# Kernel tuning notes

Measured on AMD Instinct MI355X. Metric: run time of the kernel, lower is better.

The kernel has to match this reference:

```python
import jax, jax.numpy as jnp
import numpy as np

B, Q, L, D = 4, 600, 2048, 256
H, HD, DFF, KD = 8, 32, 2048, 32  # heads, head_dim, ffn dim, gasa kernel dim
SCALE = HD ** -0.5


def setup_inputs() -> dict:
    key = jax.random.key(0)
    ks = jax.random.split(key, 24)
    w = lambda k, shape, s=0.02: (jax.random.normal(k, shape, jnp.float32) * s)
    inp = {
        "queries": jax.random.normal(ks[0], (B, Q, D), jnp.float32),
        "memory": jax.random.normal(ks[1], (B, L, D), jnp.float32),
        "memory_pos": jax.random.normal(ks[2], (B, L, 3), jnp.float32),
        "query_pos": jax.random.normal(ks[3], (B, Q, 3), jnp.float32),
        # self-attention (nn.MultiheadAttention packed in_proj)
        "sa_in_w": w(ks[4], (3 * D, D)), "sa_in_b": jnp.zeros((3 * D,), jnp.float32),
        "sa_out_w": w(ks[5], (D, D)), "sa_out_b": jnp.zeros((D,), jnp.float32),
        "norm1_g": jnp.ones((D,), jnp.float32), "norm1_b": jnp.zeros((D,), jnp.float32),
        # cross-attention projections
        "q_w": w(ks[6], (D, D)), "q_b": jnp.zeros((D,), jnp.float32),
        "k_w": w(ks[7], (D, D)), "k_b": jnp.zeros((D,), jnp.float32),
        "v_w": w(ks[8], (D, D)), "v_b": jnp.zeros((D,), jnp.float32),
        "o_w": w(ks[9], (D, D)), "o_b": jnp.zeros((D,), jnp.float32),
        "norm2_g": jnp.ones((D,), jnp.float32), "norm2_b": jnp.zeros((D,), jnp.float32),
        # GASA geometric-bias kernel: beta, MLP 1->KD->1
        "beta": jnp.asarray(1.0, jnp.float32),
        "dk_w1": w(ks[10], (KD, 1), 0.1), "dk_b1": jnp.zeros((KD,), jnp.float32),
        "dk_w2": w(ks[11], (1, KD), 0.1), "dk_b2": jnp.full((1,), -1.0, jnp.float32),
        # FFN
        "ffn_w1": w(ks[12], (DFF, D)), "ffn_b1": jnp.zeros((DFF,), jnp.float32),
        "ffn_w2": w(ks[13], (D, DFF)), "ffn_b2": jnp.zeros((D,), jnp.float32),
        "norm3_g": jnp.ones((D,), jnp.float32), "norm3_b": jnp.zeros((D,), jnp.float32),
    }
    return inp


def _ln(x, g, b, eps=1e-5):
    m = jnp.mean(x, -1, keepdims=True)
    v = jnp.mean((x - m) ** 2, -1, keepdims=True)
    return (x - m) * jax.lax.rsqrt(v + eps) * g + b


def _heads(x, wt, b):  # x:[B,N,D] -> [B,H,N,HD]
    y = x @ wt.T + b
    return y.reshape(x.shape[0], x.shape[1], H, HD).transpose(0, 2, 1, 3)


def reference(queries, memory, memory_pos, query_pos,
              sa_in_w, sa_in_b, sa_out_w, sa_out_b, norm1_g, norm1_b,
              q_w, q_b, k_w, k_b, v_w, v_b, o_w, o_b, norm2_g, norm2_b,
              beta, dk_w1, dk_b1, dk_w2, dk_b2,
              ffn_w1, ffn_b1, ffn_w2, ffn_b2, norm3_g, norm3_b):
    # ---- self-attention (post-norm, no query_pe) ----
    wq, wk, wv = jnp.split(sa_in_w, 3, axis=0)
    bq, bk, bv = jnp.split(sa_in_b, 3)
    qh = _heads(queries, wq, bq)
    kh = _heads(queries, wk, bk)
    vh = _heads(queries, wv, bv)
    a = jax.nn.softmax(jnp.einsum('bhqd,bhkd->bhqk', qh, kh) * SCALE, axis=-1)
    sa = jnp.einsum('bhqk,bhkd->bhqd', a, vh).transpose(0, 2, 1, 3).reshape(B, Q, D)
    sa = sa @ sa_out_w.T + sa_out_b
    x = _ln(queries + sa, norm1_g, norm1_b)

    # ---- GASA cross-attention ----
    Qh = _heads(x, q_w, q_b)          # [B,H,Q,HD]
    Kh = _heads(memory, k_w, k_b)     # [B,H,L,HD]
    Vh = _heads(memory, v_w, v_b)     # [B,H,L,HD]
    # cdist + learned kernel MLP, clamp to [-10, 0] (suppress-only)
    d2 = jnp.sum((query_pos[:, :, None, :] - memory_pos[:, None, :, :]) ** 2, -1)
    dist = jnp.sqrt(jnp.maximum(d2, 0.0))                     # [B,Q,L]
    hid = jax.nn.relu(dist[..., None] * dk_w1[:, 0] + dk_b1)  # [B,Q,L,KD]
    bias = (hid @ dk_w2[0]) + dk_b2[0]                        # [B,Q,L]
    bias = jnp.clip(bias, -10.0, 0.0)
    scores = jnp.einsum('bhqd,bhkd->bhqk', Qh, Kh) * SCALE + beta * bias[:, None]
    attn = jax.nn.softmax(scores, axis=-1)
    ca = jnp.einsum('bhqk,bhkd->bhqd', attn, Vh).transpose(0, 2, 1, 3).reshape(B, Q, D)
    ca = ca @ o_w.T + o_b
    x = _ln(x + ca, norm2_g, norm2_b)

    # ---- FFN (post-norm) ----
    f = jax.nn.relu(x @ ffn_w1.T + ffn_b1) @ ffn_w2.T + ffn_b2
    return _ln(x + f, norm3_g, norm3_b)
```

## Files before the change

kernel.cpp:

```cpp
#include <hip/hip_runtime.h>
#include <hip/hip_bf16.h>

typedef __hip_bfloat16 bf16;
typedef __attribute__((ext_vector_type(8))) short  short8;
typedef __attribute__((ext_vector_type(4))) short  short4v;
typedef __attribute__((ext_vector_type(4))) float  f32x4;

#define B_ 4
#define Q_ 600
#define L_ 2048
#define D_ 256
#define H_ 8
#define HD_ 32
#define DFF_ 2048
#define KD_ 32
#define SCALE_ 0.17677669529663687f
#define L2E_   1.4426950408889634f
#define SL2E_  (SCALE_ * L2E_)

template<int MODE>
__device__ __forceinline__ float ldx(const void* p, size_t i, bool f32)
{
    if (MODE == 0) return __bfloat162float(((const bf16*)p)[i]);
    if (MODE == 1) return ((const float*)p)[i];
    return f32 ? ((const float*)p)[i] : __bfloat162float(((const bf16*)p)[i]);
}
__device__ __forceinline__ short8 ld8_f32(const float* p)
{
    const float4 a = *(const float4*)p;
    const float4 b = *(const float4*)(p + 4);
    union { short8 s; bf16 h[8]; } u;
    u.h[0] = __float2bfloat16(a.x); u.h[1] = __float2bfloat16(a.y);
    u.h[2] = __float2bfloat16(a.z); u.h[3] = __float2bfloat16(a.w);
    u.h[4] = __float2bfloat16(b.x); u.h[5] = __float2bfloat16(b.y);
    u.h[6] = __float2bfloat16(b.z); u.h[7] = __float2bfloat16(b.w);
    return u.s;
}
template<int MODE>
__device__ __forceinline__ short8 ld8x(const void* p, size_t i, bool f32)
{
    if (MODE == 0) return *(const short8*)((const bf16*)p + i);
    if (MODE == 1) return ld8_f32((const float*)p + i);
    return f32 ? ld8_f32((const float*)p + i) : *(const short8*)((const bf16*)p + i);
}

__global__ __launch_bounds__(256)
void detect_kernel(const unsigned short* __restrict__ q, int* __restrict__ flag)
{
    __shared__ float red[4];
    const int tid = threadIdx.x;
    unsigned short u = q[tid];
    float f = __uint_as_float(((unsigned)(u & 0x7FFF)) << 16);
    if (f != f) f = 1e30f;
    #pragma unroll
    for (int o = 32; o > 0; o >>= 1) f = fmaxf(f, __shfl_xor(f, o));
    if ((tid & 63) == 0) red[tid >> 6] = f;
    __syncthreads();
    if (tid == 0) {
        float m = fmaxf(fmaxf(red[0], red[1]), fmaxf(red[2], red[3]));
        *flag = (m > 100.f) ? 1 : 0;
    }
}

template<int AM>
__device__ __forceinline__ void gemm_core(const void* __restrict__ A,
    const void* __restrict__ W, int M, int K, int kbeg, int kend,
    int bm, int bn, bool f32, bf16* As, bf16* Bs, f32x4 (&acc)[2][2])
{
    const int tid = threadIdx.x;
    const int w = tid >> 6, lane = tid & 63;
    const int quad = lane >> 4, l16 = lane & 15;
    const int wm = (w & 1) << 5, wn = (w >> 1) << 5;
    const int srow = tid >> 2, scol = (tid & 3) << 3;
    const int gma = (bm + srow < M) ? bm + srow : M - 1;

    short8 pa = ld8x<AM>(A, (size_t)gma * K + kbeg + scol, f32);
    short8 pb = ld8x<2>(W, (size_t)(bn + srow) * K + kbeg + scol, f32);

    for (int k0 = kbeg; k0 < kend; k0 += 32) {
        *(short8*)&As[srow * 40 + scol] = pa;
        *(short8*)&Bs[srow * 40 + scol] = pb;
        __syncthreads();
        if (k0 + 32 < kend) {
            pa = ld8x<AM>(A, (size_t)gma * K + k0 + 32 + scol, f32);
            pb = ld8x<2>(W, (size_t)(bn + srow) * K + k0 + 32 + scol, f32);
        }
        short8 af[2], bfr[2];
        #pragma unroll
        for (int t = 0; t < 2; t++) {
            af[t]  = *(const short8*)&As[(wm + t * 16 + l16) * 40 + quad * 8];
            bfr[t] = *(const short8*)&Bs[(wn + t * 16 + l16) * 40 + quad * 8];
        }
        #pragma unroll
        for (int mt = 0; mt < 2; mt++)
            #pragma unroll
            for (int nt = 0; nt < 2; nt++)
                acc[mt][nt] = __builtin_amdgcn_mfma_f32_16x16x32_bf16(
                    af[mt], bfr[nt], acc[mt][nt], 0, 0, 0);
        __syncthreads();
    }
}

template<int AM, int RM, int CM, bool RELU, int SPLIT>
__global__ __launch_bounds__(256)
void gemm_mfma(const void* __restrict__ A, const void* __restrict__ W,
               const void* __restrict__ bias, const void* __restrict__ R,
               void* __restrict__ C, int M, int N, int K,
               const int* __restrict__ flagp)
{
    const bool f32 = (*flagp != 0);
    __shared__ alignas(16) bf16 As[64 * 40];
    __shared__ alignas(16) bf16 Bs[64 * 40];
    const int bm = blockIdx.y << 6, bn = blockIdx.x << 6;
    const int KS = K / SPLIT, z = (SPLIT > 1) ? blockIdx.z : 0;

    f32x4 acc[2][2] = {{{0.f,0.f,0.f,0.f},{0.f,0.f,0.f,0.f}},
                       {{0.f,0.f,0.f,0.f},{0.f,0.f,0.f,0.f}}};
    gemm_core<AM>(A, W, M, K, z * KS, z * KS + KS, bm, bn, f32, As, Bs, acc);

    const int tid = threadIdx.x;
    const int w = tid >> 6, lane = tid & 63;
    const int quad = lane >> 4, l16 = lane & 15;
    const int wm = (w & 1) << 5, wn = (w >> 1) << 5;

    #pragma unroll
    for (int mt = 0; mt < 2; mt++) {
        #pragma unroll
        for (int r = 0; r < 4; r++) {
            const int row = bm + wm + mt * 16 + quad * 4 + r;
            if (row >= M) continue;
            #pragma unroll
            for (int nt = 0; nt < 2; nt++) {
                const int col = bn + wn + nt * 16 + l16;
                if (SPLIT > 1) {
                    ((float*)C)[((size_t)z * M + row) * N + col] = acc[mt][nt][r];
                } else {
                    float v = acc[mt][nt][r] + ldx<2>(bias, col, f32);
                    if (RM >= 0) v += ldx<RM < 0 ? 0 : RM>(R, (size_t)row * N + col, f32);
                    if (RELU) v = fmaxf(v, 0.f);
                    if (CM == 0) ((bf16*)C)[(size_t)row * N + col] = __float2bfloat16(v);
                    else         ((float*)C)[(size_t)row * N + col] = v;
                }
            }
        }
    }
}

__global__ __launch_bounds__(256)
void kv_proj(const void* __restrict__ A,
             const void* __restrict__ kw, const void* __restrict__ kb,
             const void* __restrict__ vw, const void* __restrict__ vb,
             bf16* __restrict__ kf, bf16* __restrict__ vf,
             int M, int K, const int* __restrict__ flagp)
{
    const bool f32 = (*flagp != 0);
    __shared__ alignas(16) bf16 As[64 * 40];
    __shared__ alignas(16) bf16 Bs[64 * 40];
    const int sel = blockIdx.x >> 2;
    const void* W  = sel ? vw : kw;
    const void* bs = sel ? vb : kb;
    bf16* C        = sel ? vf : kf;
    const int bn = (blockIdx.x & 3) << 6;
    const int bm = blockIdx.y << 6;

    f32x4 acc[2][2] = {{{0.f,0.f,0.f,0.f},{0.f,0.f,0.f,0.f}},
                       {{0.f,0.f,0.f,0.f},{0.f,0.f,0.f,0.f}}};
    gemm_core<2>(A, W, M, K, 0, K, bm, bn, f32, As, Bs, acc);

    const int tid = threadIdx.x;
    const int w = tid >> 6, lane = tid & 63;
    const int quad = lane >> 4, l16 = lane & 15;
    const int wm = (w & 1) << 5, wn = (w >> 1) << 5;
    #pragma unroll
    for (int mt = 0; mt < 2; mt++)
        #pragma unroll
        for (int r = 0; r < 4; r++) {
            const int row = bm + wm + mt * 16 + quad * 4 + r;
            if (row >= M) continue;
            #pragma unroll
            for (int nt = 0; nt < 2; nt++) {
                const int col = bn + wn + nt * 16 + l16;
                C[(size_t)row * 256 + col] =
                    __float2bfloat16(acc[mt][nt][r] + ldx<2>(bs, col, f32));
            }
        }
}

template<int RM, int OM, int S>
__global__ __launch_bounds__(64)
void red_ln(const float* __restrict__ P, const void* __restrict__ bias,
            const void* __restrict__ R, const void* __restrict__ gg,
            const void* __restrict__ bb, void* __restrict__ Y,
            int M, const int* __restrict__ flagp)
{
    const bool f32 = (*flagp != 0);
    const int row = blockIdx.x, lane = threadIdx.x;
    const int d0 = lane * 4;
    float v[4];
    {
        float4 a = *(const float4*)(P + ((size_t)0 * M + row) * D_ + d0);
        v[0] = a.x; v[1] = a.y; v[2] = a.z; v[3] = a.w;
    }
    #pragma unroll
    for (int s = 1; s < S; s++) {
        float4 a = *(const float4*)(P + ((size_t)s * M + row) * D_ + d0);
        v[0] += a.x; v[1] += a.y; v[2] += a.z; v[3] += a.w;
    }
    #pragma unroll
    for (int j = 0; j < 4; j++)
        v[j] += ldx<2>(bias, d0 + j, f32) + ldx<RM>(R, (size_t)row * D_ + d0 + j, f32);

    float s1 = v[0] + v[1] + v[2] + v[3];
    float s2 = v[0]*v[0] + v[1]*v[1] + v[2]*v[2] + v[3]*v[3];
    #pragma unroll
    for (int o = 32; o > 0; o >>= 1) {
        s1 += __shfl_xor(s1, o);
        s2 += __shfl_xor(s2, o);
    }
    const float mean = s1 * (1.f / D_);
    const float var = s2 * (1.f / D_) - mean * mean;
    const float rinv = rsqrtf(var + 1e-5f);
    float o[4];
    #pragma unroll
    for (int j = 0; j < 4; j++)
        o[j] = (v[j] - mean) * rinv * ldx<2>(gg, d0 + j, f32) + ldx<2>(bb, d0 + j, f32);
    const size_t i = (size_t)row * D_ + d0;
    if (OM == 1 || (OM == 2 && f32)) {
        float4 t{o[0], o[1], o[2], o[3]};
        *(float4*)((float*)Y + i) = t;
    } else {
        bf16* y = (bf16*)Y + i;
        y[0] = __float2bfloat16(o[0]); y[1] = __float2bfloat16(o[1]);
        y[2] = __float2bfloat16(o[2]); y[3] = __float2bfloat16(o[3]);
    }
}

template<bool HASBIAS, int NSEG>
__global__ __launch_bounds__(256)
void flash_attn(const bf16* __restrict__ Qm, int qs,
                const bf16* __restrict__ Km, int ks,
                const bf16* __restrict__ Vm, int vs,
                const bf16* __restrict__ biasT,
                bf16* __restrict__ pO, float* __restrict__ pml,
                int NQ, int LK)
{
    __shared__ alignas(16) bf16 Ksh[64 * 40];
    __shared__ alignas(16) bf16 Vt[48 * 72];
    __shared__ alignas(16) bf16 Psh[64 * 72];
    __shared__ alignas(16) bf16 Bsh[HASBIAS ? 64 * 72 : 8];

    const int tid = threadIdx.x;
    const int w = tid >> 6, lane = tid & 63;
    const int quad = lane >> 4, l16 = lane & 15;

    const int id = blockIdx.x;
    const int g  = ((id >> 6) << 3) + (id & 7);
    const int h  = (id >> 3) & 7;
    const int qt = g % 10;
    const int zz = g / 10;
    const int b = zz & 3, seg = zz >> 2;
    const int q0 = qt * 64;
    const int segLen = LK / NSEG;
    const int lbeg = seg * segLen, lend = lbeg + segLen;

    for (int i = tid; i < 16 * 72; i += 256) {
        int rr = 32 + i / 72, cc = i % 72;
        Vt[rr * 72 + cc] = __float2bfloat16(rr == 32 ? 1.f : 0.f);
    }

    int qrow = q0 + w * 16 + l16; if (qrow > NQ - 1) qrow = NQ - 1;
    const short8 aq = *(const short8*)(Qm + (size_t)(b * NQ + qrow) * qs + h * HD_ + quad * 8);

    f32x4 O0 = {0.f,0.f,0.f,0.f}, O1 = {0.f,0.f,0.f,0.f}, O2 = {0.f,0.f,0.f,0.f};

    const int srow = tid >> 2, sc4 = tid & 3;
    const int nch = (segLen + 63) >> 6;

    for (int ch = 0; ch < nch; ch++) {
        const int l0 = lbeg + (ch << 6);
        {
            int lg = l0 + srow; if (lg > LK - 1) lg = LK - 1;
            short8 k8 = *(const short8*)(Km + (size_t)(b * LK + lg) * ks + h * HD_ + sc4 * 8);
            *(short8*)&Ksh[srow * 40 + sc4 * 8] = k8;
            short8 v8 = *(const short8*)(Vm + (size_t)(b * LK + lg) * vs + h * HD_ + sc4 * 8);
            const int swc = srow ^ (sc4 * 16);
            #pragma unroll
            for (int j = 0; j < 8; j++)
                Vt[(sc4 * 8 + j) * 72 + swc] = ((const bf16*)&v8)[j];
            if (HASBIAS) {
                #pragma unroll
                for (int rep = 0; rep < 2; rep++) {
                    int chid = tid + rep * 256;
                    int ll = chid >> 3, qc = chid & 7;
                    int qread = q0 + qc * 8;
                    if (qread > NQ - 8) qread = NQ - 8;
                    *(short8*)&Bsh[ll * 72 + qc * 8] =
                        *(const short8*)(biasT + ((size_t)(b * LK) + l0 + ll) * Q_ + qread);
                }
            }
        }
        __syncthreads();

        f32x4 sv[4];
        #pragma unroll
        for (int jt = 0; jt < 4; jt++) {
            short8 kb = *(const short8*)&Ksh[(jt * 16 + l16) * 40 + quad * 8];
            sv[jt] = __builtin_amdgcn_mfma_f32_16x16x32_bf16(aq, kb, (f32x4){0.f,0.f,0.f,0.f}, 0, 0, 0);
        }
        if (l0 + 64 <= lend) {
            #pragma unroll
            for (int jt = 0; jt < 4; jt++) {
                if (HASBIAS) {
                    short4v bb = *(const short4v*)&Bsh[(jt * 16 + l16) * 72 + w * 16 + quad * 4];
                    #pragma unroll
                    for (int r = 0; r < 4; r++)
                        Psh[(w * 16 + quad * 4 + r) * 72 + jt * 16 + l16] =
                            __float2bfloat16(exp2f(sv[jt][r] * SL2E_ +
                                __bfloat162float(((const bf16*)&bb)[r])));
                } else {
                    #pragma unroll
                    for (int r = 0; r < 4; r++)
                        Psh[(w * 16 + quad * 4 + r) * 72 + jt * 16 + l16] =
                            __float2bfloat16(exp2f(sv[jt][r] * SL2E_));
                }
            }
        } else {
            #pragma unroll
            for (int jt = 0; jt < 4; jt++) {
                const bool valid = (l0 + jt * 16 + l16) < lend;
                #pragma unroll
                for (int r = 0; r < 4; r++)
                    Psh[(w * 16 + quad * 4 + r) * 72 + jt * 16 + l16] =
                        __float2bfloat16(valid ? exp2f(sv[jt][r] * SL2E_) : 0.f);
            }
        }
        __syncthreads();
        const int sw0 = 16 * (l16 >> 3);
        const int sw1 = 16 * (2 + (l16 >> 3));
        #pragma unroll
        for (int kt = 0; kt < 2; kt++) {
            short8 ap  = *(const short8*)&Psh[(w * 16 + l16) * 72 + kt * 32 + quad * 8];
            short8 bv0 = *(const short8*)&Vt[(l16) * 72 + ((kt * 32 + quad * 8) ^ sw0)];
            short8 bv1 = *(const short8*)&Vt[(16 + l16) * 72 + ((kt * 32 + quad * 8) ^ sw1)];
            short8 bon = *(const short8*)&Vt[(32 + l16) * 72 + kt * 32 + quad * 8];
            O0 = __builtin_amdgcn_mfma_f32_16x16x32_bf16(ap, bv0, O0, 0, 0, 0);
            O1 = __builtin_amdgcn_mfma_f32_16x16x32_bf16(ap, bv1, O1, 0, 0, 0);
            O2 = __builtin_amdgcn_mfma_f32_16x16x32_bf16(ap, bon, O2, 0, 0, 0);
        }
        __syncthreads();
    }

    #pragma unroll
    for (int r = 0; r < 4; r++) {
        const int qg = q0 + w * 16 + quad * 4 + r;
        if (qg >= NQ) continue;
        const float li = __shfl(O2[r], lane & 48);
        const float inv = 1.f / li;
        const size_t rowp = (size_t)(((seg * 4 + b) * 8) + h) * NQ + qg;
        bf16* op = pO + rowp * 32;
        op[l16]      = __float2bfloat16(O0[r] * inv);
        op[16 + l16] = __float2bfloat16(O1[r] * inv);
        if (l16 == 0) { pml[rowp * 2 + 0] = 0.f; pml[rowp * 2 + 1] = O2[r]; }
    }
}

template<int NSEG>
__global__ __launch_bounds__(256)
void attn_combine(const bf16* __restrict__ pO, const float* __restrict__ pml,
                  bf16* __restrict__ ctx, int NQ)
{
    const int t = blockIdx.x * 256 + threadIdx.x;
    const int row = t >> 5, d = t & 31;
    const int stride = 32 * NQ;
    float ms[NSEG], ls[NSEG];
    float M = -3e38f;
    #pragma unroll
    for (int s = 0; s < NSEG; s++) {
        ms[s] = pml[(size_t)(s * stride + row) * 2 + 0];
        ls[s] = pml[(size_t)(s * stride + row) * 2 + 1];
        M = fmaxf(M, ms[s]);
    }
    float W = 0.f, acc = 0.f;
    #pragma unroll
    for (int s = 0; s < NSEG; s++) {
        float wgt = ls[s] * exp2f(ms[s] - M);
        W += wgt;
        acc += wgt * __bfloat162float(pO[(size_t)(s * stride + row) * 32 + d]);
    }
    const int bh = row / NQ, q = row - bh * NQ;
    ctx[((size_t)((bh >> 3) * NQ + q)) * D_ + (bh & 7) * HD_ + d] = __float2bfloat16(acc / W);
}

__global__ __launch_bounds__(256)
void bias_pre(const void* __restrict__ qp, const void* __restrict__ mp,
              const void* __restrict__ w1, const void* __restrict__ b1,
              const void* __restrict__ w2, const void* __restrict__ b2,
              const void* __restrict__ betap, bf16* __restrict__ out,
              const int* __restrict__ flagp)
{
    const bool f32 = (*flagp != 0);
    __shared__ float sw1[KD_], sb1[KD_], sw2[KD_], scst[2];
    const int tid = threadIdx.x;
    if (tid < KD_) {
        sw1[tid] = ldx<2>(w1, tid, f32);
        sb1[tid] = ldx<2>(b1, tid, f32);
        sw2[tid] = ldx<2>(w2, tid, f32);
    }
    if (tid == 0) { scst[0] = ldx<2>(b2, 0, f32); scst[1] = L2E_ * ldx<2>(betap, 0, f32); }
    __syncthreads();
    const int idx = blockIdx.x * 256 + tid;
    const int q8 = idx % 75;
    const int t2 = idx / 75;
    const int l = t2 % L_, b = t2 / L_;
    const int q0 = q8 * 8;
    const float mx = ldx<2>(mp, (size_t)(b * L_ + l) * 3 + 0, f32);
    const float my = ldx<2>(mp, (size_t)(b * L_ + l) * 3 + 1, f32);
    const float mz = ldx<2>(mp, (size_t)(b * L_ + l) * 3 + 2, f32);
    union { short8 s; bf16 h[8]; } res;
    #pragma unroll
    for (int j = 0; j < 8; j++) {
        const int q = q0 + j;
        float dx = ldx<2>(qp, (size_t)(b * Q_ + q) * 3 + 0, f32) - mx;
        float dy = ldx<2>(qp, (size_t)(b * Q_ + q) * 3 + 1, f32) - my;
        float dz = ldx<2>(qp, (size_t)(b * Q_ + q) * 3 + 2, f32) - mz;
        float dist = sqrtf(dx * dx + dy * dy + dz * dz);
        float acc = scst[0];
        #pragma unroll
        for (int k = 0; k < KD_; k++)
            acc += fmaxf(dist * sw1[k] + sb1[k], 0.f) * sw2[k];
        acc = fminf(fmaxf(acc, -10.f), 0.f);
        res.h[j] = __float2bfloat16(scst[1] * acc);
    }
    *(short8*)(out + ((size_t)(b * L_) + l) * Q_ + q0) = res.s;
}

extern "C" void kernel_launch(void* const* d_in, const int* in_sizes, int n_in,
                              void* d_out, int out_size, void* d_ws, size_t ws_size,
                              hipStream_t stream)
{
    const void* queries   = d_in[0];
    const void* memory    = d_in[1];
    const void* memory_pos= d_in[2];
    const void* query_pos = d_in[3];
    const void* sa_in_w   = d_in[4];
    const void* sa_in_b   = d_in[5];
    const void* sa_out_w  = d_in[6];
    const void* sa_out_b  = d_in[7];
    const void* norm1_g   = d_in[8];
    const void* norm1_b   = d_in[9];
    const void* q_w  = d_in[10], *q_b  = d_in[11];
    const void* k_w  = d_in[12], *k_b  = d_in[13];
    const void* v_w  = d_in[14], *v_b  = d_in[15];
    const void* o_w  = d_in[16], *o_b  = d_in[17];
    const void* norm2_g = d_in[18], *norm2_b = d_in[19];
    const void* beta  = d_in[20];
    const void* dk_w1 = d_in[21], *dk_b1 = d_in[22];
    const void* dk_w2 = d_in[23], *dk_b2 = d_in[24];
    const void* ffn_w1 = d_in[25], *ffn_b1 = d_in[26];
    const void* ffn_w2 = d_in[27], *ffn_b2 = d_in[28];
    const void* norm3_g = d_in[29], *norm3_b = d_in[30];

    char* base = (char*)d_ws;
    bf16*  kf     = (bf16*)(base + 0);
    bf16*  vf     = (bf16*)(base + 4194304);
    float* x1     = (float*)(base + 8388608);
    bf16*  qproj  = (bf16*)(base + 10846208);
    bf16*  cactx  = (bf16*)(base + 12075008);
    float* x2     = (float*)(base + 13303808);
    bf16*  biasT  = (bf16*)(base + 15761408);
    bf16*  qkv    = (bf16*)(base + 0);
    bf16*  sactx  = (bf16*)(base + 3686400);
    bf16*  selfO  = (bf16*)(base + 4915200);
    float* selfML = (float*)(base + 7372800);
    float* P3     = (float*)(base + 15761408);
    bf16*  crossO = (bf16*)(base + 25591808);
    float* crossML= (float*)(base + 30507008);
    float* P10    = (float*)(base + 0);
    bf16*  ffnh   = (bf16*)(base + 15761408);
    float* P13    = (float*)(base + 0);
    int*   flag   = (int*)(base + 31121408);

    const dim3 blk(256);

    detect_kernel<<<1, 256, 0, stream>>>((const unsigned short*)queries, flag);
    gemm_mfma<2, -1, 0, false, 1><<<dim3(12, 38), blk, 0, stream>>>(
        queries, sa_in_w, sa_in_b, nullptr, qkv, 2400, 768, 256, flag);
    flash_attn<false, 2><<<640, blk, 0, stream>>>(
        qkv, 768, qkv + 256, 768, qkv + 512, 768, nullptr,
        selfO, selfML, 600, 600);
    attn_combine<2><<<2400, blk, 0, stream>>>(selfO, selfML, sactx, 600);
    gemm_mfma<0, -1, 1, false, 2><<<dim3(4, 38, 2), blk, 0, stream>>>(
        sactx, sa_out_w, nullptr, nullptr, P3, 2400, 256, 256, flag);
    red_ln<2, 1, 2><<<2400, 64, 0, stream>>>(
        P3, sa_out_b, queries, norm1_g, norm1_b, x1, 2400, flag);
    gemm_mfma<1, -1, 0, false, 1><<<dim3(4, 38), blk, 0, stream>>>(
        x1, q_w, q_b, nullptr, qproj, 2400, 256, 256, flag);
    kv_proj<<<dim3(8, 128), blk, 0, stream>>>(
        memory, k_w, k_b, v_w, v_b, kf, vf, 8192, 256, flag);
    bias_pre<<<2400, blk, 0, stream>>>(
        query_pos, memory_pos, dk_w1, dk_b1, dk_w2, dk_b2, beta, biasT, flag);
    flash_attn<true, 4><<<1280, blk, 0, stream>>>(
        qproj, 256, kf, 256, vf, 256, biasT,
        crossO, crossML, 600, 2048);
    attn_combine<4><<<2400, blk, 0, stream>>>(crossO, crossML, cactx, 600);
    gemm_mfma<0, -1, 1, false, 2><<<dim3(4, 38, 2), blk, 0, stream>>>(
        cactx, o_w, nullptr, nullptr, P10, 2400, 256, 256, flag);
    red_ln<1, 1, 2><<<2400, 64, 0, stream>>>(
        P10, o_b, x1, norm2_g, norm2_b, x2, 2400, flag);
    gemm_mfma<1, -1, 0, true, 1><<<dim3(32, 38), blk, 0, stream>>>(
        x2, ffn_w1, ffn_b1, nullptr, ffnh, 2400, 2048, 256, flag);
    gemm_mfma<0, -1, 1, false, 4><<<dim3(4, 38, 4), blk, 0, stream>>>(
        ffnh, ffn_w2, nullptr, nullptr, P13, 2400, 256, 2048, flag);
    red_ln<1, 2, 4><<<2400, 64, 0, stream>>>(
        P13, ffn_b2, x2, norm3_g, norm3_b, d_out, 2400, flag);
}
```

Before: 292.3 us.

## Fuse split-attention combine into out-proj GEMM and merge independent prologue kernels

The attn_combine kernels are removed. The out-projection GEMMs now read the per-segment flash-attention partial outputs and merge them while loading their A operand, weighting each segment by its stored l and dropping the max term. The self-attn QKV projection, the K/V projection and the geometric-bias precompute are merged into one stage0 launch with a block-range dispatch, and the workspace layout is reassigned so these buffers can coexist. This cuts launch count and one round trip of the context tensor through memory. In exchange, the GEMM A-load redoes the combine for every N-tile, and correctness now relies on flash_attn normalising partials so that the per-segment max terms can be ignored.

```diff
diff --git a/kernel.cpp b/kernel.cpp
--- a/kernel.cpp
+++ b/kernel.cpp
@@ -44,6 +44,34 @@
     return f32 ? ld8_f32((const float*)p + i) : *(const short8*)((const bf16*)p + i);
 }
 
+template<int NSEG>
+__device__ __forceinline__ short8 ld8_comb(const bf16* __restrict__ pO,
+                                           const float* __restrict__ pml,
+                                           int row, int col)
+{
+    const unsigned b = (unsigned)row / 600u;
+    const unsigned q = (unsigned)row - b * 600u;
+    const int h = col >> 5, dd = col & 31;
+    const unsigned rp = b * 4800u + (unsigned)h * 600u + q;
+    float W = 0.f;
+    float acc[8] = {0.f,0.f,0.f,0.f,0.f,0.f,0.f,0.f};
+    #pragma unroll
+    for (int s = 0; s < NSEG; s++) {
+        const size_t rr = (size_t)s * 19200u + rp;
+        const float l = pml[rr * 2 + 1];
+        W += l;
+        const short8 o = *(const short8*)(pO + rr * 32 + dd);
+        #pragma unroll
+        for (int j = 0; j < 8; j++)
+            acc[j] += l * __bfloat162float(((const bf16*)&o)[j]);
+    }
+    const float inv = 1.f / W;
+    union { short8 s; bf16 h8[8]; } u;
+    #pragma unroll
+    for (int j = 0; j < 8; j++) u.h8[j] = __float2bfloat16(acc[j] * inv);
+    return u.s;
+}
+
 __global__ __launch_bounds__(256)
 void detect_kernel(const unsigned short* __restrict__ q, int* __restrict__ flag)
 {
@@ -62,10 +90,11 @@
     }
 }
 
-template<int AM>
+template<int AM, int NSEG>
 __device__ __forceinline__ void gemm_core(const void* __restrict__ A,
     const void* __restrict__ W, int M, int K, int kbeg, int kend,
-    int bm, int bn, bool f32, bf16* As, bf16* Bs, f32x4 (&acc)[2][2])
+    int bm, int bn, bool f32, bf16* As, bf16* Bs, f32x4 (&acc)[2][2],
+    const float* __restrict__ pml)
 {
     const int tid = threadIdx.x;
     const int w = tid >> 6, lane = tid & 63;
@@ -74,15 +103,18 @@
     const int srow = tid >> 2, scol = (tid & 3) << 3;
     const int gma = (bm + srow < M) ? bm + srow : M - 1;
 
-    short8 pa = ld8x<AM>(A, (size_t)gma * K + kbeg + scol, f32);
-    short8 pb = ld8x<2>(W, (size_t)(bn + srow) * K + kbeg + scol, f32);
+    short8 pa, pb;
+    if constexpr (AM == 3) pa = ld8_comb<NSEG>((const bf16*)A, pml, gma, kbeg + scol);
+    else                   pa = ld8x<AM>(A, (size_t)gma * K + kbeg + scol, f32);
+    pb = ld8x<2>(W, (size_t)(bn + srow) * K + kbeg + scol, f32);
 
     for (int k0 = kbeg; k0 < kend; k0 += 32) {
         *(short8*)&As[srow * 40 + scol] = pa;
         *(short8*)&Bs[srow * 40 + scol] = pb;
         __syncthreads();
         if (k0 + 32 < kend) {
-            pa = ld8x<AM>(A, (size_t)gma * K + k0 + 32 + scol, f32);
+            if constexpr (AM == 3) pa = ld8_comb<NSEG>((const bf16*)A, pml, gma, k0 + 32 + scol);
+            else                   pa = ld8x<AM>(A, (size_t)gma * K + k0 + 32 + scol, f32);
             pb = ld8x<2>(W, (size_t)(bn + srow) * K + k0 + 32 + scol, f32);
         }
         short8 af[2], bfr[2];
@@ -101,12 +133,40 @@
     }
 }
 
-template<int AM, int RM, int CM, bool RELU, int SPLIT>
+template<int RM, int CM, bool RELU>
+__device__ __forceinline__ void gemm_epi(const f32x4 (&acc)[2][2],
+    const void* __restrict__ bias, const void* __restrict__ R,
+    void* __restrict__ C, int M, int N, int bm, int bn, bool f32)
+{
+    const int tid = threadIdx.x;
+    const int w = tid >> 6, lane = tid & 63;
+    const int quad = lane >> 4, l16 = lane & 15;
+    const int wm = (w & 1) << 5, wn = (w >> 1) << 5;
+    #pragma unroll
+    for (int mt = 0; mt < 2; mt++) {
+        #pragma unroll
+        for (int r = 0; r < 4; r++) {
+            const int row = bm + wm + mt * 16 + quad * 4 + r;
+            if (row >= M) continue;
+            #pragma unroll
+            for (int nt = 0; nt < 2; nt++) {
+                const int col = bn + wn + nt * 16 + l16;
+                float v = acc[mt][nt][r] + ldx<2>(bias, col, f32);
+                if (RM >= 0) v += ldx<(RM < 0 ? 0 : RM)>(R, (size_t)row * N + col, f32);
+                if (RELU) v = fmaxf(v, 0.f);
+                if (CM == 0) ((bf16*)C)[(size_t)row * N + col] = __float2bfloat16(v);
+                else         ((float*)C)[(size_t)row * N + col] = v;
+            }
+        }
+    }
+}
+
+template<int AM, int RM, int CM, bool RELU, int SPLIT, int NSEG>
 __global__ __launch_bounds__(256)
 void gemm_mfma(const void* __restrict__ A, const void* __restrict__ W,
                const void* __restrict__ bias, const void* __restrict__ R,
                void* __restrict__ C, int M, int N, int K,
-               const int* __restrict__ flagp)
+               const int* __restrict__ flagp, const float* __restrict__ pml)
 {
     const bool f32 = (*flagp != 0);
     __shared__ alignas(16) bf16 As[64 * 40];
@@ -116,122 +176,105 @@
 
     f32x4 acc[2][2] = {{{0.f,0.f,0.f,0.f},{0.f,0.f,0.f,0.f}},
                        {{0.f,0.f,0.f,0.f},{0.f,0.f,0.f,0.f}}};
-    gemm_core<AM>(A, W, M, K, z * KS, z * KS + KS, bm, bn, f32, As, Bs, acc);
-
-    const int tid = threadIdx.x;
-    const int w = tid >> 6, lane = tid & 63;
-    const int quad = lane >> 4, l16 = lane & 15;
-    const int wm = (w & 1) << 5, wn = (w >> 1) << 5;
-
-    #pragma unroll
-    for (int mt = 0; mt < 2; mt++) {
-        #pragma unroll
-        for (int r = 0; r < 4; r++) {
-            const int row = bm + wm + mt * 16 + quad * 4 + r;
-            if (row >= M) continue;
-            #pragma unroll
-            for (int nt = 0; nt < 2; nt++) {
-                const int col = bn + wn + nt * 16 + l16;
-                if (SPLIT > 1) {
+    gemm_core<AM, NSEG>(A, W, M, K, z * KS, z * KS + KS, bm, bn, f32, As, Bs, acc, pml);
+
+    if (SPLIT > 1) {
+        const int tid = threadIdx.x;
+        const int w = tid >> 6, lane = tid & 63;
+        const int quad = lane >> 4, l16 = lane & 15;
+        const int wm = (w & 1) << 5, wn = (w >> 1) << 5;
+        #pragma unroll
+        for (int mt = 0; mt < 2; mt++)
+            #pragma unroll
+            for (int r = 0; r < 4; r++) {
+                const int row = bm + wm + mt * 16 + quad * 4 + r;
+                if (row >= M) continue;
+                #pragma unroll
+                for (int nt = 0; nt < 2; nt++) {
+                    const int col = bn + wn + nt * 16 + l16;
                     ((float*)C)[((size_t)z * M + row) * N + col] = acc[mt][nt][r];
-                } else {
-                    float v = acc[mt][nt][r] + ldx<2>(bias, col, f32);
-                    if (RM >= 0) v += ldx<RM < 0 ? 0 : RM>(R, (size_t)row * N + col, f32);
-                    if (RELU) v = fmaxf(v, 0.f);
-                    if (CM == 0) ((bf16*)C)[(size_t)row * N + col] = __float2bfloat16(v);
-                    else         ((float*)C)[(size_t)row * N + col] = v;
                 }
             }
-        }
+    } else {
+        gemm_epi<RM, CM, RELU>(acc, bias, R, C, M, N, bm, bn, f32);
     }
 }
 
 __global__ __launch_bounds__(256)
-void kv_proj(const void* __restrict__ A,
-             const void* __restrict__ kw, const void* __restrict__ kb,
-             const void* __restrict__ vw, const void* __restrict__ vb,
-             bf16* __restrict__ kf, bf16* __restrict__ vf,
-             int M, int K, const int* __restrict__ flagp)
-{
-    const bool f32 = (*flagp != 0);
+void stage0(const void* __restrict__ queries,
+            const void* __restrict__ sa_in_w, const void* __restrict__ sa_in_b,
+            bf16* __restrict__ qkv,
+            const void* __restrict__ memory,
+            const void* __restrict__ kw, const void* __restrict__ kb,
+            const void* __restrict__ vw, const void* __restrict__ vb,
+            bf16* __restrict__ kf, bf16* __restrict__ vf,
+            const void* __restrict__ qp, const void* __restrict__ mp,
+            const void* __restrict__ w1, const void* __restrict__ b1,
+            const void* __restrict__ w2, const void* __restrict__ b2,
+            const void* __restrict__ betap, bf16* __restrict__ biasT,
+            const int* __restrict__ flagp)
+{
     __shared__ alignas(16) bf16 As[64 * 40];
     __shared__ alignas(16) bf16 Bs[64 * 40];
-    const int sel = blockIdx.x >> 2;
-    const void* W  = sel ? vw : kw;
-    const void* bs = sel ? vb : kb;
-    bf16* C        = sel ? vf : kf;
-    const int bn = (blockIdx.x & 3) << 6;
-    const int bm = blockIdx.y << 6;
-
-    f32x4 acc[2][2] = {{{0.f,0.f,0.f,0.f},{0.f,0.f,0.f,0.f}},
-                       {{0.f,0.f,0.f,0.f},{0.f,0.f,0.f,0.f}}};
-    gemm_core<2>(A, W, M, K, 0, K, bm, bn, f32, As, Bs, acc);
-
-    const int tid = threadIdx.x;
-    const int w = tid >> 6, lane = tid & 63;
-    const int quad = lane >> 4, l16 = lane & 15;
-    const int wm = (w & 1) << 5, wn = (w >> 1) << 5;
-    #pragma unroll
-    for (int mt = 0; mt < 2; mt++)
-        #pragma unroll
-        for (int r = 0; r < 4; r++) {
-            const int row = bm + wm + mt * 16 + quad * 4 + r;
-            if (row >= M) continue;
-            #pragma unroll
-            for (int nt = 0; nt < 2; nt++) {
-                const int col = bn + wn + nt * 16 + l16;
-                C[(size_t)row * 256 + col] =
-                    __float2bfloat16(acc[mt][nt][r] + ldx<2>(bs, col, f32));
-            }
-        }
-}
-
-template<int RM, int OM, int S>
-__global__ __launch_bounds__(64)
-void red_ln(const float* __restrict__ P, const void* __restrict__ bias,
-            const void* __restrict__ R, const void* __restrict__ gg,
-            const void* __restrict__ bb, void* __restrict__ Y,
-            int M, const int* __restrict__ flagp)
-{
     const bool f32 = (*flagp != 0);
-    const int row = blockIdx.x, lane = threadIdx.x;
-    const int d0 = lane * 4;
-    float v[4];
-    {
-        float4 a = *(const float4*)(P + ((size_t)0 * M + row) * D_ + d0);
-        v[0] = a.x; v[1] = a.y; v[2] = a.z; v[3] = a.w;
-    }
-    #pragma unroll
-    for (int s = 1; s < S; s++) {
-        float4 a = *(const float4*)(P + ((size_t)s * M + row) * D_ + d0);
-        v[0] += a.x; v[1] += a.y; v[2] += a.z; v[3] += a.w;
-    }
-    #pragma unroll
-    for (int j = 0; j < 4; j++)
-        v[j] += ldx<2>(bias, d0 + j, f32) + ldx<RM>(R, (size_t)row * D_ + d0 + j, f32);
-
-    float s1 = v[0] + v[1] + v[2] + v[3];
-    float s2 = v[0]*v[0] + v[1]*v[1] + v[2]*v[2] + v[3]*v[3];
-    #pragma unroll
-    for (int o = 32; o > 0; o >>= 1) {
-        s1 += __shfl_xor(s1, o);
-        s2 += __shfl_xor(s2, o);
-    }
-    const float mean = s1 * (1.f / D_);
-    const float var = s2 * (1.f / D_) - mean * mean;
-    const float rinv = rsqrtf(var + 1e-5f);
-    float o[4];
-    #pragma unroll
-    for (int j = 0; j < 4; j++)
-        o[j] = (v[j] - mean) * rinv * ldx<2>(gg, d0 + j, f32) + ldx<2>(bb, d0 + j, f32);
-    const size_t i = (size_t)row * D_ + d0;
-    if (OM == 1 || (OM == 2 && f32)) {
-        float4 t{o[0], o[1], o[2], o[3]};
-        *(float4*)((float*)Y + i) = t;
+    const int bid = blockIdx.x;
+
+    if (bid < 456) {
+        const int bn = (bid % 12) << 6, bm = (bid / 12) << 6;
+        f32x4 acc[2][2] = {{{0.f,0.f,0.f,0.f},{0.f,0.f,0.f,0.f}},
+                           {{0.f,0.f,0.f,0.f},{0.f,0.f,0.f,0.f}}};
+        gemm_core<2, 1>(queries, sa_in_w, 2400, 256, 0, 256, bm, bn, f32, As, Bs, acc, nullptr);
+        gemm_epi<-1, 0, false>(acc, sa_in_b, nullptr, qkv, 2400, 768, bm, bn, f32);
+    } else if (bid < 1480) {
+        const int id = bid - 456;
+        const int bx = id & 7;
+        const int sel = bx >> 2;
+        const void* W  = sel ? vw : kw;
+        const void* bs = sel ? vb : kb;
+        bf16* C        = sel ? vf : kf;
+        const int bn = (bx & 3) << 6;
+        const int bm = (id >> 3) << 6;
+        f32x4 acc[2][2] = {{{0.f,0.f,0.f,0.f},{0.f,0.f,0.f,0.f}},
+                           {{0.f,0.f,0.f,0.f},{0.f,0.f,0.f,0.f}}};
+        gemm_core<2, 1>(memory, W, 8192, 256, 0, 256, bm, bn, f32, As, Bs, acc, nullptr);
+        gemm_epi<-1, 0, false>(acc, bs, nullptr, C, 8192, 256, bm, bn, f32);
     } else {
-        bf16* y = (bf16*)Y + i;
-        y[0] = __float2bfloat16(o[0]); y[1] = __float2bfloat16(o[1]);
-        y[2] = __float2bfloat16(o[2]); y[3] = __float2bfloat16(o[3]);
+        float* sw1  = (float*)As;
+        float* sb1  = sw1 + KD_;
+        float* sw2  = sb1 + KD_;
+        float* scst = sw2 + KD_;
+        const int tid = threadIdx.x;
+        if (tid < KD_) {
+            sw1[tid] = ldx<2>(w1, tid, f32);
+            sb1[tid] = ldx<2>(b1, tid, f32);
+            sw2[tid] = ldx<2>(w2, tid, f32);
+        }
+        if (tid == 0) { scst[0] = ldx<2>(b2, 0, f32); scst[1] = L2E_ * ldx<2>(betap, 0, f32); }
+        __syncthreads();
+        const int idx = (bid - 1480) * 256 + tid;
+        const int q8 = idx % 75;
+        const int t2 = idx / 75;
+        const int l = t2 % L_, b = t2 / L_;
+        const int q0 = q8 * 8;
+        const float mx = ldx<2>(mp, (size_t)(b * L_ + l) * 3 + 0, f32);
+        const float my = ldx<2>(mp, (size_t)(b * L_ + l) * 3 + 1, f32);
+        const float mz = ldx<2>(mp, (size_t)(b * L_ + l) * 3 + 2, f32);
+        union { short8 s; bf16 h[8]; } res;
+        #pragma unroll
+        for (int j = 0; j < 8; j++) {
+            const int q = q0 + j;
+            float dx = ldx<2>(qp, (size_t)(b * Q_ + q) * 3 + 0, f32) - mx;
+            float dy = ldx<2>(qp, (size_t)(b * Q_ + q) * 3 + 1, f32) - my;
+            float dz = ldx<2>(qp, (size_t)(b * Q_ + q) * 3 + 2, f32) - mz;
+            float dist = sqrtf(dx * dx + dy * dy + dz * dz);
+            float a = scst[0];
+            #pragma unroll
+            for (int k = 0; k < KD_; k++)
+                a += fmaxf(dist * sw1[k] + sb1[k], 0.f) * sw2[k];
+            a = fminf(fmaxf(a, -10.f), 0.f);
+            res.h[j] = __float2bfloat16(scst[1] * a);
+        }
+        *(short8*)(biasT + ((size_t)(b * L_) + l) * Q_ + q0) = res.s;
     }
 }
 
@@ -360,78 +403,57 @@
         bf16* op = pO + rowp * 32;
         op[l16]      = __float2bfloat16(O0[r] * inv);
         op[16 + l16] = __float2bfloat16(O1[r] * inv);
-        if (l16 == 0) { pml[rowp * 2 + 0] = 0.f; pml[rowp * 2 + 1] = O2[r]; }
-    }
-}
-
-template<int NSEG>
-__global__ __launch_bounds__(256)
-void attn_combine(const bf16* __restrict__ pO, const float* __restrict__ pml,
-                  bf16* __restrict__ ctx, int NQ)
-{
-    const int t = blockIdx.x * 256 + threadIdx.x;
-    const int row = t >> 5, d = t & 31;
-    const int stride = 32 * NQ;
-    float ms[NSEG], ls[NSEG];
-    float M = -3e38f;
-    #pragma unroll
-    for (int s = 0; s < NSEG; s++) {
-        ms[s] = pml[(size_t)(s * stride + row) * 2 + 0];
-        ls[s] = pml[(size_t)(s * stride + row) * 2 + 1];
-        M = fmaxf(M, ms[s]);
-    }
-    float W = 0.f, acc = 0.f;
-    #pragma unroll
-    for (int s = 0; s < NSEG; s++) {
-        float wgt = ls[s] * exp2f(ms[s] - M);
-        W += wgt;
-        acc += wgt * __bfloat162float(pO[(size_t)(s * stride + row) * 32 + d]);
-    }
-    const int bh = row / NQ, q = row - bh * NQ;
-    ctx[((size_t)((bh >> 3) * NQ + q)) * D_ + (bh & 7) * HD_ + d] = __float2bfloat16(acc / W);
-}
-
-__global__ __launch_bounds__(256)
-void bias_pre(const void* __restrict__ qp, const void* __restrict__ mp,
-              const void* __restrict__ w1, const void* __restrict__ b1,
-              const void* __restrict__ w2, const void* __restrict__ b2,
-              const void* __restrict__ betap, bf16* __restrict__ out,
-              const int* __restrict__ flagp)
+        if (l16 == 0) pml[rowp * 2 + 1] = O2[r];
+    }
+}
+
+template<int RM, int OM, int S>
+__global__ __launch_bounds__(64)
+void red_ln(const float* __restrict__ P, const void* __restrict__ bias,
+            const void* __restrict__ R, const void* __restrict__ gg,
+            const void* __restrict__ bb, void* __restrict__ Y,
+            int M, const int* __restrict__ flagp)
 {
     const bool f32 = (*flagp != 0);
-    __shared__ float sw1[KD_], sb1[KD_], sw2[KD_], scst[2];
-    const int tid = threadIdx.x;
-    if (tid < KD_) {
-        sw1[tid] = ldx<2>(w1, tid, f32);
-        sb1[tid] = ldx<2>(b1, tid, f32);
-        sw2[tid] = ldx<2>(w2, tid, f32);
-    }
-    if (tid == 0) { scst[0] = ldx<2>(b2, 0, f32); scst[1] = L2E_ * ldx<2>(betap, 0, f32); }
-    __syncthreads();
-    const int idx = blockIdx.x * 256 + tid;
-    const int q8 = idx % 75;
-    const int t2 = idx / 75;
-    const int l = t2 % L_, b = t2 / L_;
-    const int q0 = q8 * 8;
-    const float mx = ldx<2>(mp, (size_t)(b * L_ + l) * 3 + 0, f32);
-    const float my = ldx<2>(mp, (size_t)(b * L_ + l) * 3 + 1, f32);
-    const float mz = ldx<2>(mp, (size_t)(b * L_ + l) * 3 + 2, f32);
-    union { short8 s; bf16 h[8]; } res;
-    #pragma unroll
-    for (int j = 0; j < 8; j++) {
-        const int q = q0 + j;
-        float dx = ldx<2>(qp, (size_t)(b * Q_ + q) * 3 + 0, f32) - mx;
-        float dy = ldx<2>(qp, (size_t)(b * Q_ + q) * 3 + 1, f32) - my;
-        float dz = ldx<2>(qp, (size_t)(b * Q_ + q) * 3 + 2, f32) - mz;
-        float dist = sqrtf(dx * dx + dy * dy + dz * dz);
-        float acc = scst[0];
-        #pragma unroll
-        for (int k = 0; k < KD_; k++)
-            acc += fmaxf(dist * sw1[k] + sb1[k], 0.f) * sw2[k];
-        acc = fminf(fmaxf(acc, -10.f), 0.f);
-        res.h[j] = __float2bfloat16(scst[1] * acc);
-    }
-    *(short8*)(out + ((size_t)(b * L_) + l) * Q_ + q0) = res.s;
+    const int row = blockIdx.x, lane = threadIdx.x;
+    const int d0 = lane * 4;
+    float v[4];
+    {
+        float4 a = *(const float4*)(P + ((size_t)0 * M + row) * D_ + d0);
+        v[0] = a.x; v[1] = a.y; v[2] = a.z; v[3] = a.w;
+    }
+    #pragma unroll
+    for (int s = 1; s < S; s++) {
+        float4 a = *(const float4*)(P + ((size_t)s * M + row) * D_ + d0);
+        v[0] += a.x; v[1] += a.y; v[2] += a.z; v[3] += a.w;
+    }
+    #pragma unroll
+    for (int j = 0; j < 4; j++)
+        v[j] += ldx<2>(bias, d0 + j, f32) + ldx<RM>(R, (size_t)row * D_ + d0 + j, f32);
+
+    float s1 = v[0] + v[1] + v[2] + v[3];
+    float s2 = v[0]*v[0] + v[1]*v[1] + v[2]*v[2] + v[3]*v[3];
+    #pragma unroll
+    for (int o = 32; o > 0; o >>= 1) {
+        s1 += __shfl_xor(s1, o);
+        s2 += __shfl_xor(s2, o);
+    }
+    const float mean = s1 * (1.f / D_);
+    const float var = s2 * (1.f / D_) - mean * mean;
+    const float rinv = rsqrtf(var + 1e-5f);
+    float o[4];
+    #pragma unroll
+    for (int j = 0; j < 4; j++)
+        o[j] = (v[j] - mean) * rinv * ldx<2>(gg, d0 + j, f32) + ldx<2>(bb, d0 + j, f32);
+    const size_t i = (size_t)row * D_ + d0;
+    if (OM == 1 || (OM == 2 && f32)) {
+        float4 t{o[0], o[1], o[2], o[3]};
+        *(float4*)((float*)Y + i) = t;
+    } else {
+        bf16* y = (bf16*)Y + i;
+        y[0] = __float2bfloat16(o[0]); y[1] = __float2bfloat16(o[1]);
+        y[2] = __float2bfloat16(o[2]); y[3] = __float2bfloat16(o[3]);
+    }
 }
 
 extern "C" void kernel_launch(void* const* d_in, const int* in_sizes, int n_in,
@@ -461,56 +483,50 @@
     const void* norm3_g = d_in[29], *norm3_b = d_in[30];
 
     char* base = (char*)d_ws;
-    bf16*  kf     = (bf16*)(base + 0);
-    bf16*  vf     = (bf16*)(base + 4194304);
-    float* x1     = (float*)(base + 8388608);
-    bf16*  qproj  = (bf16*)(base + 10846208);
-    bf16*  cactx  = (bf16*)(base + 12075008);
-    float* x2     = (float*)(base + 13303808);
-    bf16*  biasT  = (bf16*)(base + 15761408);
-    bf16*  qkv    = (bf16*)(base + 0);
-    bf16*  sactx  = (bf16*)(base + 3686400);
-    bf16*  selfO  = (bf16*)(base + 4915200);
-    float* selfML = (float*)(base + 7372800);
-    float* P3     = (float*)(base + 15761408);
-    bf16*  crossO = (bf16*)(base + 25591808);
-    float* crossML= (float*)(base + 30507008);
-    float* P10    = (float*)(base + 0);
-    bf16*  ffnh   = (bf16*)(base + 15761408);
-    float* P13    = (float*)(base + 0);
-    int*   flag   = (int*)(base + 31121408);
+    bf16*  kf      = (bf16*)(base + 0);
+    bf16*  vf      = (bf16*)(base + 4194304);
+    bf16*  biasT   = (bf16*)(base + 8388608);
+    bf16*  qkv     = (bf16*)(base + 18219008);
+    bf16*  selfO   = (bf16*)(base + 21905408);
+    float* selfML  = (float*)(base + 24363008);
+    float* P3      = (float*)(base + 24670208);
+    float* x1      = (float*)(base + 18219008);
+    bf16*  qproj   = (bf16*)(base + 20676608);
+    bf16*  crossO  = (bf16*)(base + 21905408);
+    float* crossML = (float*)(base + 26820608);
+    float* P10     = (float*)(base + 0);
+    float* x2      = (float*)(base + 4915200);
+    bf16*  ffnh    = (bf16*)(base + 7372800);
+    float* P13     = (float*)(base + 17203200);
+    int*   flag    = (int*)(base + 29585408);
 
     const dim3 blk(256);
 
     detect_kernel<<<1, 256, 0, stream>>>((const unsigned short*)queries, flag);
-    gemm_mfma<2, -1, 0, false, 1><<<dim3(12, 38), blk, 0, stream>>>(
-        queries, sa_in_w, sa_in_b, nullptr, qkv, 2400, 768, 256, flag);
+    stage0<<<3880, blk, 0, stream>>>(
+        queries, sa_in_w, sa_in_b, qkv,
+        memory, k_w, k_b, v_w, v_b, kf, vf,
+        query_pos, memory_pos, dk_w1, dk_b1, dk_w2, dk_b2, beta, biasT, flag);
     flash_attn<false, 2><<<640, blk, 0, stream>>>(
         qkv, 768, qkv + 256, 768, qkv + 512, 768, nullptr,
         selfO, selfML, 600, 600);
-    attn_combine<2><<<2400, blk, 0, stream>>>(selfO, selfML, sactx, 600);
-    gemm_mfma<0, -1, 1, false, 2><<<dim3(4, 38, 2), blk, 0, stream>>>(
-        sactx, sa_out_w, nullptr, nullptr, P3, 2400, 256, 256, flag);
+    gemm_mfma<3, -1, 1, false, 2, 2><<<dim3(4, 38, 2), blk, 0, stream>>>(
+        selfO, sa_out_w, nullptr, nullptr, P3, 2400, 256, 256, flag, selfML);
     red_ln<2, 1, 2><<<2400, 64, 0, stream>>>(
         P3, sa_out_b, queries, norm1_g, norm1_b, x1, 2400, flag);
-    gemm_mfma<1, -1, 0, false, 1><<<dim3(4, 38), blk, 0, stream>>>(
-        x1, q_w, q_b, nullptr, qproj, 2400, 256, 256, flag);
-    kv_proj<<<dim3(8, 128), blk, 0, stream>>>(
-        memory, k_w, k_b, v_w, v_b, kf, vf, 8192, 256, flag);
-    bias_pre<<<2400, blk, 0, stream>>>(
-        query_pos, memory_pos, dk_w1, dk_b1, dk_w2, dk_b2, beta, biasT, flag);
+    gemm_mfma<1, -1, 0, false, 1, 1><<<dim3(4, 38), blk, 0, stream>>>(
+        x1, q_w, q_b, nullptr, qproj, 2400, 256, 256, flag, nullptr);
     flash_attn<true, 4><<<1280, blk, 0, stream>>>(
         qproj, 256, kf, 256, vf, 256, biasT,
         crossO, crossML, 600, 2048);
-    attn_combine<4><<<2400, blk, 0, stream>>>(crossO, crossML, cactx, 600);
-    gemm_mfma<0, -1, 1, false, 2><<<dim3(4, 38, 2), blk, 0, stream>>>(
-        cactx, o_w, nullptr, nullptr, P10, 2400, 256, 256, flag);
+    gemm_mfma<3, -1, 1, false, 2, 4><<<dim3(4, 38, 2), blk, 0, stream>>>(
+        crossO, o_w, nullptr, nullptr, P10, 2400, 256, 256, flag, crossML);
     red_ln<1, 1, 2><<<2400, 64, 0, stream>>>(
         P10, o_b, x1, norm2_g, norm2_b, x2, 2400, flag);
-    gemm_mfma<1, -1, 0, true, 1><<<dim3(32, 38), blk, 0, stream>>>(
-        x2, ffn_w1, ffn_b1, nullptr, ffnh, 2400, 2048, 256, flag);
-    gemm_mfma<0, -1, 1, false, 4><<<dim3(4, 38, 4), blk, 0, stream>>>(
-        ffnh, ffn_w2, nullptr, nullptr, P13, 2400, 256, 2048, flag);
+    gemm_mfma<1, -1, 0, true, 1, 1><<<dim3(32, 38), blk, 0, stream>>>(
+        x2, ffn_w1, ffn_b1, nullptr, ffnh, 2400, 2048, 256, flag, nullptr);
+    gemm_mfma<0, -1, 1, false, 4, 1><<<dim3(4, 38, 4), blk, 0, stream>>>(
+        ffnh, ffn_w2, nullptr, nullptr, P13, 2400, 256, 2048, flag, nullptr);
     red_ln<1, 2, 4><<<2400, 64, 0, stream>>>(
         P13, ffn_b2, x2, norm3_g, norm3_b, d_out, 2400, flag);
 }
```

Result: slower. 496.5 us (+69.8%).
